# Kernel tuning notes

Hardware: AMD Instinct MI355X
Metric: run time of the kernel (lower is better)

Reference implementation:

```python
import jax, jax.numpy as jnp
import numpy as np

DEPTH = 6


def sparsemax(z):
    # sparsemax along last axis (matches tfa.activations.sparsemax default axis=-1)
    d = z.shape[-1]
    z_sorted = -jnp.sort(-z, axis=-1)                      # descending
    cs = jnp.cumsum(z_sorted, axis=-1)
    k = jnp.arange(1, d + 1, dtype=z.dtype)
    support = z_sorted * k > (cs - 1.0)
    k_sup = jnp.sum(support, axis=-1, keepdims=True)       # size of support
    cs_k = jnp.take_along_axis(cs, k_sup.astype(jnp.int32) - 1, axis=-1)
    tau = (cs_k - 1.0) / k_sup.astype(z.dtype)
    return jnp.maximum(z - tau, 0.0)


def binary_lut(depth):
    # (depth, 2^depth, 2): bit s of each leaf code and its complement
    idx = jnp.arange(2 ** depth)
    off = 2 ** jnp.arange(depth)
    bits = (idx[None, :] // off[:, None]) % 2
    return jnp.stack([bits, 1 - bits], axis=-1).astype(jnp.float32)


def setup_inputs() -> dict:
    key = jax.random.key(0)
    ks = jax.random.split(key, 5)
    batch, dim, n_trees, depth, units = 1024, 256, 512, DEPTH, 16
    return {
        "x": jax.random.normal(ks[0], (batch, dim), dtype=jnp.float32),
        "feature_selection_logits": jax.random.normal(ks[1], (dim, n_trees, depth), dtype=jnp.float32),
        "feature_thresholds": jax.random.normal(ks[2], (n_trees, depth), dtype=jnp.float32) * 0.1,
        "log_temperatures": jax.random.normal(ks[3], (n_trees, depth), dtype=jnp.float32) * 0.1,
        "response": jax.random.normal(ks[4], (n_trees, units, 2 ** depth), dtype=jnp.float32),
    }


def reference(x, feature_selection_logits, feature_thresholds, log_temperatures, response):
    lut = binary_lut(DEPTH)                                     # (d, c, 2)
    selectors = sparsemax(feature_selection_logits)             # (i, n, d)
    fv = jnp.einsum('bi,ind->bnd', x, selectors)                # (b, n, d)
    tl = (fv - feature_thresholds) * jnp.exp(-log_temperatures) # (b, n, d)
    tl2 = jnp.stack([-tl, tl], axis=-1)                         # (b, n, d, 2)
    gates = jnp.clip(0.5 * tl2 + 0.5, 0.0, 1.0)                 # sparsemoid
    rg = jnp.einsum('bnds,dcs->bndc', gates, lut)               # (b, n, d, 2^d)
    rg = jnp.prod(rg, axis=-2)                                  # (b, n, 2^d)
    out = jnp.einsum('bnc,nuc->bnu', rg, response)              # (b, n, u)
    return jnp.mean(out, axis=1)                                # (b, u)
```

## Files before the change

### kernel.cpp

```cpp
#include <hip/hip_runtime.h>
#include <hip/hip_bf16.h>

#define DEPTH   6
#define NLEAF   64
#define BATCH   1024
#define DIM     256
#define NTREES  512
#define UNITS   16
#define NCOLS   (NTREES*DEPTH)

#define GROWS 32
#define GCOLS 128
#define GKCH  32

#define TPT   4
#define NTG   (NTREES/TPT)

#define WS_GATES 0
#define WS_THRP  (WS_GATES + BATCH*NCOLS)
#define WS_SH    (WS_THRP + NCOLS)

__global__ void prep_kernel(const float* __restrict__ fsl,
                            const float* __restrict__ thr,
                            const float* __restrict__ lt,
                            float* __restrict__ selp,
                            float* __restrict__ thrp) {
    if (blockIdx.x == (DIM * NTREES) / 256) {
        for (int j = threadIdx.x; j < NCOLS; j += 256)
            thrp[j] = thr[j] * __expf(-lt[j]);
        return;
    }
    int t = blockIdx.x * 256 + threadIdx.x;
    int n = t & (NTREES - 1);
    int base = t * DEPTH;

    float zv[DEPTH], zs[DEPTH];
#pragma unroll
    for (int d = 0; d < DEPTH; ++d) { zv[d] = fsl[base + d]; zs[d] = zv[d]; }

#pragma unroll
    for (int p = 0; p < DEPTH - 1; ++p)
#pragma unroll
        for (int j = 0; j < DEPTH - 1 - p; ++j) {
            float a = zs[j], b = zs[j + 1];
            zs[j] = fmaxf(a, b); zs[j + 1] = fminf(a, b);
        }

    float cs[DEPTH];
    cs[0] = zs[0];
#pragma unroll
    for (int d = 1; d < DEPTH; ++d) cs[d] = cs[d - 1] + zs[d];

    int k = 0;
#pragma unroll
    for (int d = 0; d < DEPTH; ++d)
        if (zs[d] * (float)(d + 1) > cs[d] - 1.0f) k++;

    float csk = cs[0];
#pragma unroll
    for (int d = 0; d < DEPTH; ++d) csk = (k - 1 == d) ? cs[d] : csk;
    float tau = (csk - 1.0f) / (float)k;

#pragma unroll
    for (int d = 0; d < DEPTH; ++d) {
        float it = __expf(-lt[n * DEPTH + d]);
        selp[base + d] = fmaxf(zv[d] - tau, 0.0f) * it;
    }
}

__global__ void gemm_gates(const float* __restrict__ x,
                           const float* __restrict__ selp,
                           const float* __restrict__ thrp,
                           float* __restrict__ gates) {
    const int tid  = threadIdx.x;
    const int lane = tid & 63;
    const int w    = __builtin_amdgcn_readfirstlane(tid >> 6);
    const int m0   = blockIdx.x * GROWS + (w >> 1) * 16;
    const int col  = blockIdx.y * GCOLS + (w & 1) * 64 + lane;

    float acc[16];
#pragma unroll
    for (int r = 0; r < 16; ++r) acc[r] = 0.0f;

    for (int kc = 0; kc < DIM; kc += GKCH) {
        float b[GKCH];
#pragma unroll
        for (int k = 0; k < GKCH; ++k)
            b[k] = selp[(size_t)(kc + k) * NCOLS + col];

#pragma unroll
        for (int r = 0; r < 16; ++r) {
            const float* ap = &x[(size_t)(m0 + r) * DIM + kc];
#pragma unroll
            for (int k = 0; k < GKCH; ++k)
                acc[r] = fmaf(ap[k], b[k], acc[r]);
        }
    }

    const float th = thrp[col];
#pragma unroll
    for (int r = 0; r < 16; ++r) {
        float tl = acc[r] - th;
        float g  = fminf(fmaxf(fmaf(0.5f, tl, 0.5f), 0.0f), 1.0f);
        gates[(size_t)(m0 + r) * NCOLS + col] = g;
    }
}

__global__ __launch_bounds__(256, 2)
void tree_kernel(const float* __restrict__ gates,
                 const float* __restrict__ resp,
                 float* __restrict__ partial) {
    const int bid  = blockIdx.x;
    const int bc   = bid & 7;
    const int tg   = bid >> 3;
    const int tid  = threadIdx.x;
    const int uh   = __builtin_amdgcn_readfirstlane((tid >> 6) & 1);
    const int b    = bc * 128 + (tid >> 7) * 64 + (tid & 63);

    const float* gp = gates + (size_t)b * NCOLS + tg * (TPT * DEPTH);

    float out8[8];
#pragma unroll
    for (int u = 0; u < 8; ++u) out8[u] = 0.0f;

#pragma unroll
    for (int t = 0; t < TPT; ++t) {
        float g[DEPTH];
#pragma unroll
        for (int i = 0; i < 3; ++i)
            *(float2*)&g[i * 2] = *(const float2*)&gp[t * DEPTH + i * 2];

        float p[NLEAF];
        p[0] = 1.0f;
#pragma unroll
        for (int d = 0; d < DEPTH; ++d) {
            int w = 1 << d;
            float gd = g[d], hd = 1.0f - gd;
#pragma unroll
            for (int c = w - 1; c >= 0; --c) {
                float base = p[c];
                p[c + w] = base * hd;
                p[c]     = base * gd;
            }
        }

        const float4* rp4 = (const float4*)(resp +
            (size_t)((tg * TPT + t) * UNITS + uh * 8) * NLEAF);
#pragma unroll
        for (int u = 0; u < 8; ++u) {
            float s0 = 0.0f, s1 = 0.0f;
#pragma unroll
            for (int c4 = 0; c4 < 16; c4 += 2) {
                float4 r0 = rp4[u * 16 + c4];
                float4 r1 = rp4[u * 16 + c4 + 1];
                s0 = fmaf(p[c4 * 4 + 0], r0.x, s0);
                s0 = fmaf(p[c4 * 4 + 1], r0.y, s0);
                s0 = fmaf(p[c4 * 4 + 2], r0.z, s0);
                s0 = fmaf(p[c4 * 4 + 3], r0.w, s0);
                s1 = fmaf(p[c4 * 4 + 4], r1.x, s1);
                s1 = fmaf(p[c4 * 4 + 5], r1.y, s1);
                s1 = fmaf(p[c4 * 4 + 6], r1.z, s1);
                s1 = fmaf(p[c4 * 4 + 7], r1.w, s1);
            }
            out8[u] += s0 + s1;
        }
    }

    float* pp = partial + ((size_t)tg * BATCH + b) * UNITS + uh * 8;
    *(float4*)&pp[0] = *(float4*)&out8[0];
    *(float4*)&pp[4] = *(float4*)&out8[4];
}

__global__ void reduce_kernel(const float* __restrict__ partial,
                              float* __restrict__ out) {
    int idx = blockIdx.x * 256 + threadIdx.x;
    float s = 0.0f;
#pragma unroll 16
    for (int tg = 0; tg < NTG; ++tg)
        s += partial[(size_t)tg * BATCH * UNITS + idx];
    out[idx] = s * (1.0f / (float)NTREES);
}

extern "C" void kernel_launch(void* const* d_in, const int* in_sizes, int n_in,
                              void* d_out, int out_size, void* d_ws, size_t ws_size,
                              hipStream_t stream) {
    const float* x    = (const float*)d_in[0];
    const float* fsl  = (const float*)d_in[1];
    const float* thr  = (const float*)d_in[2];
    const float* lt   = (const float*)d_in[3];
    const float* resp = (const float*)d_in[4];
    float* out = (float*)d_out;
    float* ws  = (float*)d_ws;

    float* gates   = ws + WS_GATES;
    float* thrp    = ws + WS_THRP;
    float* selp    = ws + WS_SH;
    float* partial = ws + WS_SH;

    prep_kernel<<<(DIM * NTREES) / 256 + 1, 256, 0, stream>>>(fsl, thr, lt, selp, thrp);
    gemm_gates<<<dim3(BATCH / GROWS, NCOLS / GCOLS), 256, 0, stream>>>(x, selp, thrp, gates);
    tree_kernel<<<NTG * 8, 256, 0, stream>>>(gates, resp, partial);
    reduce_kernel<<<(BATCH * UNITS) / 256, 256, 0, stream>>>(partial, out);
}
```

Before: 191.8 us.

## Double-buffer selector loads in gate GEMM and stage tree responses in LDS

The gate GEMM now loads the selector matrix in 16-deep chunks with two register buffers, so the next chunk is fetched while FMAs run on the current one. It also gets launch bounds of 3 blocks per SM. The tree kernel copies its 4-tree response slice (16 KB) into shared memory once per block and reads it from LDS instead of global or scalar memory. The cost is extra LDS use and a block barrier, plus register pressure from the double buffer.

```diff
diff --git a/kernel.cpp b/kernel.cpp
--- a/kernel.cpp
+++ b/kernel.cpp
@@ -9,12 +9,13 @@
 #define UNITS   16
 #define NCOLS   (NTREES*DEPTH)
 
+#define GKC   16
 #define GROWS 32
 #define GCOLS 128
-#define GKCH  32
 
 #define TPT   4
 #define NTG   (NTREES/TPT)
+#define RLSZ  (TPT*UNITS*NLEAF)
 
 #define WS_GATES 0
 #define WS_THRP  (WS_GATES + BATCH*NCOLS)
@@ -68,10 +69,11 @@
     }
 }
 
-__global__ void gemm_gates(const float* __restrict__ x,
-                           const float* __restrict__ selp,
-                           const float* __restrict__ thrp,
-                           float* __restrict__ gates) {
+__global__ __launch_bounds__(256, 3)
+void gemm_gates(const float* __restrict__ x,
+                const float* __restrict__ selp,
+                const float* __restrict__ thrp,
+                float* __restrict__ gates) {
     const int tid  = threadIdx.x;
     const int lane = tid & 63;
     const int w    = __builtin_amdgcn_readfirstlane(tid >> 6);
@@ -82,20 +84,30 @@
 #pragma unroll
     for (int r = 0; r < 16; ++r) acc[r] = 0.0f;
 
-    for (int kc = 0; kc < DIM; kc += GKCH) {
-        float b[GKCH];
-#pragma unroll
-        for (int k = 0; k < GKCH; ++k)
-            b[k] = selp[(size_t)(kc + k) * NCOLS + col];
-
-#pragma unroll
-        for (int r = 0; r < 16; ++r) {
-            const float* ap = &x[(size_t)(m0 + r) * DIM + kc];
-#pragma unroll
-            for (int k = 0; k < GKCH; ++k)
-                acc[r] = fmaf(ap[k], b[k], acc[r]);
-        }
-    }
+    float bA[GKC], bB[GKC];
+
+#define LOADB(B_, KC_)                                                         \
+    _Pragma("unroll")                                                          \
+    for (int k = 0; k < GKC; ++k)                                              \
+        B_[k] = selp[(size_t)((KC_) * GKC + k) * NCOLS + col];
+#define FMAS(B_, KC_)                                                          \
+    _Pragma("unroll")                                                          \
+    for (int r = 0; r < 16; ++r) {                                             \
+        const float* ap = &x[(size_t)(m0 + r) * DIM + (KC_) * GKC];            \
+        _Pragma("unroll")                                                      \
+        for (int k = 0; k < GKC; ++k)                                          \
+            acc[r] = fmaf(ap[k], B_[k], acc[r]);                               \
+    }
+
+    LOADB(bA, 0)
+    for (int kc = 0; kc < DIM / GKC; kc += 2) {
+        LOADB(bB, kc + 1)
+        FMAS(bA, kc)
+        if (kc + 2 < DIM / GKC) LOADB(bA, kc + 2)
+        FMAS(bB, kc + 1)
+    }
+#undef LOADB
+#undef FMAS
 
     const float th = thrp[col];
 #pragma unroll
@@ -110,6 +122,8 @@
 void tree_kernel(const float* __restrict__ gates,
                  const float* __restrict__ resp,
                  float* __restrict__ partial) {
+    __shared__ float rl[RLSZ];
+
     const int bid  = blockIdx.x;
     const int bc   = bid & 7;
     const int tg   = bid >> 3;
@@ -117,6 +131,15 @@
     const int uh   = __builtin_amdgcn_readfirstlane((tid >> 6) & 1);
     const int b    = bc * 128 + (tid >> 7) * 64 + (tid & 63);
 
+    {
+        const float4* rg = (const float4*)(resp + (size_t)tg * RLSZ);
+        float4* rl4 = (float4*)rl;
+#pragma unroll
+        for (int i = 0; i < RLSZ / 4 / 256; ++i)
+            rl4[tid + i * 256] = rg[tid + i * 256];
+    }
+    __syncthreads();
+
     const float* gp = gates + (size_t)b * NCOLS + tg * (TPT * DEPTH);
 
     float out8[8];
@@ -144,15 +167,14 @@
             }
         }
 
-        const float4* rp4 = (const float4*)(resp +
-            (size_t)((tg * TPT + t) * UNITS + uh * 8) * NLEAF);
 #pragma unroll
         for (int u = 0; u < 8; ++u) {
+            const float* rp = &rl[(t * UNITS + uh * 8 + u) * NLEAF];
             float s0 = 0.0f, s1 = 0.0f;
 #pragma unroll
             for (int c4 = 0; c4 < 16; c4 += 2) {
-                float4 r0 = rp4[u * 16 + c4];
-                float4 r1 = rp4[u * 16 + c4 + 1];
+                float4 r0 = *(const float4*)&rp[c4 * 4];
+                float4 r1 = *(const float4*)&rp[c4 * 4 + 4];
                 s0 = fmaf(p[c4 * 4 + 0], r0.x, s0);
                 s0 = fmaf(p[c4 * 4 + 1], r0.y, s0);
                 s0 = fmaf(p[c4 * 4 + 2], r0.z, s0);
```

Result: faster. 180.5 us (-5.9%).
